# Kernel tuning notes

Hardware: AMD Instinct MI355X
Metric: run time of the kernel (lower is better)

Reference implementation:

```python
import jax, jax.numpy as jnp
import numpy as np

B, S, F, P, D, H, L, FF, R = 64, 4096, 8, 16, 512, 8, 6, 2048, 8
NP = (S - P) // P + 1  # 256 patches (stride == patch_length)
DK = D // H
LORA_SCALING = 16.0 / 8.0  # lora_alpha / lora_rank


def setup_inputs() -> dict:
    key = jax.random.key(0)
    ks = iter(jax.random.split(key, 40))
    def nrm(shape, s=0.02):
        return jax.random.normal(next(ks), shape, jnp.float32) * s
    inp = {
        "x": jax.random.normal(next(ks), (B, S, F), jnp.float32),
        "patch_w": nrm((P * F, D)), "patch_b": jnp.zeros((D,), jnp.float32),
        "patch_ln_w": jnp.ones((D,), jnp.float32), "patch_ln_b": jnp.zeros((D,), jnp.float32),
        "pos_enc": nrm((1, NP, D)),
        "ln1_w": jnp.ones((L, D), jnp.float32), "ln1_b": jnp.zeros((L, D), jnp.float32),
        "q_w": nrm((L, D, D)), "q_b": jnp.zeros((L, D), jnp.float32),
        "k_w": nrm((L, D, D)), "k_b": jnp.zeros((L, D), jnp.float32),
        "v_w": nrm((L, D, D)), "v_b": jnp.zeros((L, D), jnp.float32),
        "lq_down": nrm((L, D, R)), "lq_up": nrm((L, R, D)),
        "lk_down": nrm((L, D, R)), "lk_up": nrm((L, R, D)),
        "lv_down": nrm((L, D, R)), "lv_up": nrm((L, R, D)),
        "o_w": nrm((L, D, D)), "o_b": jnp.zeros((L, D), jnp.float32),
        "ln2_w": jnp.ones((L, D), jnp.float32), "ln2_b": jnp.zeros((L, D), jnp.float32),
        "ff1_w": nrm((L, D, FF)), "ff1_b": jnp.zeros((L, FF), jnp.float32),
        "ff2_w": nrm((L, FF, D)), "ff2_b": jnp.zeros((L, D), jnp.float32),
        "norm_w": jnp.ones((D,), jnp.float32), "norm_b": jnp.zeros((D,), jnp.float32),
    }
    return inp


def _layer_norm(x, w, b):
    m = jnp.mean(x, -1, keepdims=True)
    v = jnp.mean(jnp.square(x - m), -1, keepdims=True)
    return (x - m) * jax.lax.rsqrt(v + 1e-5) * w + b


def _forward(x, patch_w, patch_b, patch_ln_w, patch_ln_b, pos_enc,
             ln1_w, ln1_b, q_w, q_b, k_w, k_b, v_w, v_b,
             lq_down, lq_up, lk_down, lk_up, lv_down, lv_up,
             o_w, o_b, ln2_w, ln2_b, ff1_w, ff1_b, ff2_w, ff2_b,
             norm_w, norm_b):
    # Patch embedding: [B,S,F] -> [B,F,S] -> unfold(stride==patch) -> [B,NP,F*P]
    patches = x.transpose(0, 2, 1).reshape(B, F, NP, P).transpose(0, 2, 1, 3).reshape(B, NP, F * P)
    h = _layer_norm(patches @ patch_w + patch_b, patch_ln_w, patch_ln_b) + pos_enc
    inv_scale = 1.0 / np.sqrt(DK).astype(np.float32)
    for i in range(L):
        y = _layer_norm(h, ln1_w[i], ln1_b[i])
        q = y @ q_w[i] + q_b[i] + (y @ lq_down[i]) @ lq_up[i] * LORA_SCALING
        k = y @ k_w[i] + k_b[i] + (y @ lk_down[i]) @ lk_up[i] * LORA_SCALING
        v = y @ v_w[i] + v_b[i] + (y @ lv_down[i]) @ lv_up[i] * LORA_SCALING
        q = q.reshape(B, NP, H, DK)
        k = k.reshape(B, NP, H, DK)
        v = v.reshape(B, NP, H, DK)
        scores = jnp.einsum('bqhd,bkhd->bhqk', q, k) * inv_scale
        probs = jax.nn.softmax(scores, axis=-1)
        attn = jnp.einsum('bhqk,bkhd->bqhd', probs, v).reshape(B, NP, D)
        h = h + attn @ o_w[i] + o_b[i]
        y = _layer_norm(h, ln2_w[i], ln2_b[i])
        ff = jax.nn.gelu(y @ ff1_w[i] + ff1_b[i], approximate=False) @ ff2_w[i] + ff2_b[i]
        h = h + ff
    h = _layer_norm(h, norm_w, norm_b)
    return h.mean(axis=1)  # [B, D]


def reference(x, patch_w, patch_b, patch_ln_w, patch_ln_b, pos_enc,
              ln1_w, ln1_b, q_w, q_b, k_w, k_b, v_w, v_b,
              lq_down, lq_up, lk_down, lk_up, lv_down, lv_up,
              o_w, o_b, ln2_w, ln2_b, ff1_w, ff1_b, ff2_w, ff2_b,
              norm_w, norm_b):
    return _forward(x, patch_w, patch_b, patch_ln_w, patch_ln_b, pos_enc,
                    ln1_w, ln1_b, q_w, q_b, k_w, k_b, v_w, v_b,
                    lq_down, lq_up, lk_down, lk_up, lv_down, lv_up,
                    o_w, o_b, ln2_w, ln2_b, ff1_w, ff1_b, ff2_w, ff2_b,
                    norm_w, norm_b)
```

## Files before the change

### kernel.cpp

```cpp
#include <hip/hip_runtime.h>
#include <cstdint>
#include <cstddef>

constexpr int BATCH = 64, SEQ = 4096, FEAT = 8, PLEN = 16;
constexpr int DMODEL = 512, NHEAD = 8, NLAYER = 6, DFF = 2048;
constexpr int NPATCH = 256, MROWS = BATCH * NPATCH;
constexpr int DK = 64;
constexpr int LDSP = 72;

typedef unsigned short u16t;
typedef __bf16 bf16t;
typedef bf16t bf16x8 __attribute__((ext_vector_type(8)));
typedef short s16x4 __attribute__((ext_vector_type(4)));
typedef float f32x4 __attribute__((ext_vector_type(4)));

__device__ __forceinline__ float b2f(u16t u) {
  union { unsigned int ui; float f; } v; v.ui = ((unsigned int)u) << 16; return v.f;
}
__device__ __forceinline__ u16t f2b(float f) {
  union { float f; unsigned int ui; } v; v.f = f;
  return (u16t)((v.ui + 0x7fffu + ((v.ui >> 16) & 1u)) >> 16);
}
__device__ __forceinline__ void g2l16(void* lds, const void* g) {
  __builtin_amdgcn_global_load_lds(
      (__attribute__((address_space(1))) void*)g,
      (__attribute__((address_space(3))) void*)lds, 16, 0, 0);
}

__device__ __forceinline__ float gelu_erf(float x) {
  const float z = fabsf(x) * 0.70710678118654752f;
  const float t = __builtin_amdgcn_rcpf(__builtin_fmaf(0.3275911f, z, 1.0f));
  float p = __builtin_fmaf(1.061405429f, t, -1.453152027f);
  p = __builtin_fmaf(p, t, 1.421413741f);
  p = __builtin_fmaf(p, t, -0.284496736f);
  p = __builtin_fmaf(p, t, 0.254829592f);
  const float e = __expf(-z * z);
  const float er = __builtin_fmaf(-p * t, e, 1.0f);
  const float s = copysignf(er, x);
  return 0.5f * x * (1.0f + s);
}

__global__ __launch_bounds__(256, 3) void k_gemm(
    const u16t* __restrict__ A, const u16t* __restrict__ Bt,
    const float* __restrict__ bias, const float* __restrict__ b2,
    const float* __restrict__ b3, float* __restrict__ Cf,
    u16t* __restrict__ Cb, int M, int N, int K, int mode)
{
  __shared__ __align__(16) u16t SH[3 * 8192];

  const int nbn = N >> 7;
  const int cpx = gridDim.x >> 3;
  const int wgid = (blockIdx.x & 7) * cpx + (blockIdx.x >> 3);
  const int bm = (wgid / nbn) << 7;
  const int bn = (wgid % nbn) << 7;

  const int tid = threadIdx.x, wave = tid >> 6, lane = tid & 63;
  const int lr = lane & 15, quad = lane >> 4;
  const int wm = (wave >> 1) << 6;
  const int wn = (wave & 1) << 6;

  const int sseg = (lane & 3) ^ ((lane >> 3) & 3);
  const u16t* gA = A + (size_t)(bm + (lane >> 2)) * K + sseg * 8;
  const u16t* gB = Bt + (size_t)(bn + (lane >> 2)) * K + sseg * 8;

  const int sw8 = (quad ^ ((lr >> 1) & 3)) << 3;
  const int aoff = (wm + lr) * 32 + sw8;
  const int boff = 4096 + (wn + lr) * 32 + sw8;

  f32x4 acc[4][4] = {};

  u16t* buf0 = SH;
  u16t* buf1 = SH + 8192;
  u16t* buf2 = SH + 16384;

#define STAGE(BUF_, S_) do {                                                   \
    g2l16((BUF_) + wave * 512,        gA + (size_t)(wave * 16) * K + (S_) * 32);   \
    g2l16((BUF_) + (wave + 4) * 512,  gA + (size_t)((wave + 4) * 16) * K + (S_) * 32); \
    g2l16((BUF_) + 4096 + wave * 512, gB + (size_t)(wave * 16) * K + (S_) * 32);   \
    g2l16((BUF_) + 4096 + (wave + 4) * 512, gB + (size_t)((wave + 4) * 16) * K + (S_) * 32); \
  } while (0)

  const int nt = K >> 5;
  STAGE(buf0, 0);
  STAGE(buf1, 1);

  for (int t = 0; t < nt - 1; ++t) {
    asm volatile("s_waitcnt vmcnt(4)" ::: "memory");
    __builtin_amdgcn_s_barrier();
    asm volatile("" ::: "memory");
    if (t + 2 < nt) STAGE(buf2, t + 2);
    bf16x8 af[4], bfr[4];
    #pragma unroll
    for (int i = 0; i < 4; ++i) af[i] = *(const bf16x8*)&buf0[aoff + i * 512];
    #pragma unroll
    for (int j = 0; j < 4; ++j) bfr[j] = *(const bf16x8*)&buf0[boff + j * 512];
    __builtin_amdgcn_s_setprio(1);
    #pragma unroll
    for (int j = 0; j < 4; ++j)
      #pragma unroll
      for (int i = 0; i < 4; ++i)
        acc[j][i] = __builtin_amdgcn_mfma_f32_16x16x32_bf16(bfr[j], af[i], acc[j][i], 0, 0, 0);
    __builtin_amdgcn_s_setprio(0);
    u16t* tmp = buf0; buf0 = buf1; buf1 = buf2; buf2 = tmp;
  }
  {
    asm volatile("s_waitcnt vmcnt(0)" ::: "memory");
    __builtin_amdgcn_s_barrier();
    asm volatile("" ::: "memory");
    bf16x8 af[4], bfr[4];
    #pragma unroll
    for (int i = 0; i < 4; ++i) af[i] = *(const bf16x8*)&buf0[aoff + i * 512];
    #pragma unroll
    for (int j = 0; j < 4; ++j) bfr[j] = *(const bf16x8*)&buf0[boff + j * 512];
    __builtin_amdgcn_s_setprio(1);
    #pragma unroll
    for (int j = 0; j < 4; ++j)
      #pragma unroll
      for (int i = 0; i < 4; ++i)
        acc[j][i] = __builtin_amdgcn_mfma_f32_16x16x32_bf16(bfr[j], af[i], acc[j][i], 0, 0, 0);
    __builtin_amdgcn_s_setprio(0);
  }
#undef STAGE

  const float* bp = bias;
  int reg0 = 0;
  if (bias && b2) { reg0 = (bn >> 9) << 9; bp = reg0 == 0 ? bias : (reg0 == 512 ? b2 : b3); }
  float4 bv[4];
  #pragma unroll
  for (int jN = 0; jN < 4; ++jN) {
    const int gn0 = bn + wn + jN * 16 + quad * 4;
    bv[jN] = bias ? *(const float4*)&bp[gn0 - reg0] : make_float4(0.f, 0.f, 0.f, 0.f);
  }

  if (mode <= 1) {
    __syncthreads();
    u16t* E = SH;
    #pragma unroll
    for (int jN = 0; jN < 4; ++jN) {
      const int cl = wn + jN * 16 + quad * 4;
      const int seg = cl >> 3, intra = cl & 7;
      #pragma unroll
      for (int iM = 0; iM < 4; ++iM) {
        const int r = wm + iM * 16 + lr;
        float v0 = acc[jN][iM][0] + bv[jN].x, v1 = acc[jN][iM][1] + bv[jN].y;
        float v2 = acc[jN][iM][2] + bv[jN].z, v3 = acc[jN][iM][3] + bv[jN].w;
        union { u16t h[4]; uint2 u; } pk;
        if (mode == 1) {
          pk.h[0] = f2b(gelu_erf(v0)); pk.h[1] = f2b(gelu_erf(v1));
          pk.h[2] = f2b(gelu_erf(v2)); pk.h[3] = f2b(gelu_erf(v3));
        } else {
          pk.h[0] = f2b(v0); pk.h[1] = f2b(v1); pk.h[2] = f2b(v2); pk.h[3] = f2b(v3);
        }
        *(uint2*)&E[r * 128 + ((seg ^ (r & 7)) << 3) + intra] = pk.u;
      }
    }
    __syncthreads();
    const int rr = tid >> 2, s0 = tid & 3;
    #pragma unroll
    for (int pass = 0; pass < 2; ++pass) {
      const int r = pass * 64 + rr;
      u16t* gout = Cb + (size_t)(bm + r) * N + bn;
      #pragma unroll
      for (int it = 0; it < 4; ++it) {
        const int s = s0 + it * 4;
        uint4 u = *(const uint4*)&E[r * 128 + ((s ^ (r & 7)) << 3)];
        *(uint4*)(gout + s * 8) = u;
      }
    }
  } else {
    #pragma unroll
    for (int jN = 0; jN < 4; ++jN) {
      const int gn0 = bn + wn + jN * 16 + quad * 4;
      #pragma unroll
      for (int iM = 0; iM < 4; ++iM) {
        const int gm = bm + wm + iM * 16 + lr;
        const size_t off = (size_t)gm * N + gn0;
        float v0 = acc[jN][iM][0] + bv[jN].x, v1 = acc[jN][iM][1] + bv[jN].y;
        float v2 = acc[jN][iM][2] + bv[jN].z, v3 = acc[jN][iM][3] + bv[jN].w;
        if (mode == 2) {
          float4 c = *(float4*)(Cf + off);
          c.x += v0; c.y += v1; c.z += v2; c.w += v3;
          *(float4*)(Cf + off) = c;
        } else {
          *(float4*)(Cf + off) = make_float4(v0, v1, v2, v3);
        }
      }
    }
  }
}

__global__ __launch_bounds__(256) void k_prep_w(
    const float* __restrict__ W, const float* __restrict__ down,
    const float* __restrict__ up, u16t* __restrict__ Wt, int K, int N,
    size_t ostride, int orow0)
{
  __shared__ float t[32][33];
  const int z = blockIdx.z;
  const float* Wz = W + (size_t)z * K * N;
  u16t* Wtz = Wt + (size_t)z * ostride + (size_t)orow0 * K;
  const int k0 = blockIdx.x * 32, n0 = blockIdx.y * 32;
  const int tx = threadIdx.x & 31, ty = threadIdx.x >> 5;
  for (int i = ty; i < 32; i += 8) {
    const int kk = k0 + i, nn = n0 + tx;
    float v = Wz[(size_t)kk * N + nn];
    if (down) {
      const float* dz = down + (size_t)z * K * 8 + (size_t)kk * 8;
      const float* uz = up + (size_t)z * 8 * N + nn;
      float lv = 0.f;
      #pragma unroll
      for (int r = 0; r < 8; ++r) lv += dz[r] * uz[(size_t)r * N];
      v += 2.0f * lv;
    }
    t[i][tx] = v;
  }
  __syncthreads();
  for (int i = ty; i < 32; i += 8)
    Wtz[(size_t)(n0 + i) * K + k0 + tx] = f2b(t[tx][i]);
}

__global__ void k_patch(const float* __restrict__ x, u16t* __restrict__ pt) {
  const int idx = blockIdx.x * 256 + threadIdx.x;
  const int col = idx & 127, row = idx >> 7;
  const int f = col >> 4, pp = col & 15;
  const int b = row >> 8, np = row & 255;
  pt[idx] = f2b(x[(((size_t)b << 12) + np * 16 + pp) * 8 + f]);
}

__global__ __launch_bounds__(256) void k_ln(
    const float* __restrict__ xin, const float* __restrict__ w,
    const float* __restrict__ bb, u16t* __restrict__ y)
{
  const int row = blockIdx.x * 4 + (threadIdx.x >> 6);
  const int lane = threadIdx.x & 63;
  const float4* xr = (const float4*)(xin + (size_t)row * 512);
  float4 a = xr[lane * 2], c = xr[lane * 2 + 1];
  float s = a.x + a.y + a.z + a.w + c.x + c.y + c.z + c.w;
  float qq = a.x * a.x + a.y * a.y + a.z * a.z + a.w * a.w +
             c.x * c.x + c.y * c.y + c.z * c.z + c.w * c.w;
  #pragma unroll
  for (int o = 32; o > 0; o >>= 1) { s += __shfl_xor(s, o); qq += __shfl_xor(qq, o); }
  const float mean = s * (1.f / 512.f);
  const float rs = rsqrtf(qq * (1.f / 512.f) - mean * mean + 1e-5f);
  const float4* wr = (const float4*)w; const float4* br = (const float4*)bb;
  float4 w0 = wr[lane * 2], w1 = wr[lane * 2 + 1];
  float4 b0 = br[lane * 2], b1 = br[lane * 2 + 1];
  union { u16t h[8]; uint4 v; } pk;
  pk.h[0] = f2b((a.x - mean) * rs * w0.x + b0.x);
  pk.h[1] = f2b((a.y - mean) * rs * w0.y + b0.y);
  pk.h[2] = f2b((a.z - mean) * rs * w0.z + b0.z);
  pk.h[3] = f2b((a.w - mean) * rs * w0.w + b0.w);
  pk.h[4] = f2b((c.x - mean) * rs * w1.x + b1.x);
  pk.h[5] = f2b((c.y - mean) * rs * w1.y + b1.y);
  pk.h[6] = f2b((c.z - mean) * rs * w1.z + b1.z);
  pk.h[7] = f2b((c.w - mean) * rs * w1.w + b1.w);
  *(uint4*)(y + (size_t)row * 512 + lane * 8) = pk.v;
}

__global__ __launch_bounds__(256) void k_ln_pos(
    const float* __restrict__ xin, const float* __restrict__ w,
    const float* __restrict__ bb, const float* __restrict__ pos,
    float* __restrict__ h)
{
  const int row = blockIdx.x * 4 + (threadIdx.x >> 6);
  const int lane = threadIdx.x & 63;
  const float4* xr = (const float4*)(xin + (size_t)row * 512);
  float4 a = xr[lane * 2], c = xr[lane * 2 + 1];
  float s = a.x + a.y + a.z + a.w + c.x + c.y + c.z + c.w;
  float qq = a.x * a.x + a.y * a.y + a.z * a.z + a.w * a.w +
             c.x * c.x + c.y * c.y + c.z * c.z + c.w * c.w;
  #pragma unroll
  for (int o = 32; o > 0; o >>= 1) { s += __shfl_xor(s, o); qq += __shfl_xor(qq, o); }
  const float mean = s * (1.f / 512.f);
  const float rs = rsqrtf(qq * (1.f / 512.f) - mean * mean + 1e-5f);
  const float4* wr = (const float4*)w; const float4* br = (const float4*)bb;
  float4 w0 = wr[lane * 2], w1 = wr[lane * 2 + 1];
  float4 b0 = br[lane * 2], b1 = br[lane * 2 + 1];
  const int np = row & 255;
  const float4* pr = (const float4*)(pos + (size_t)np * 512);
  float4 p0 = pr[lane * 2], p1 = pr[lane * 2 + 1];
  float4 o0, o1;
  o0.x = (a.x - mean) * rs * w0.x + b0.x + p0.x;
  o0.y = (a.y - mean) * rs * w0.y + b0.y + p0.y;
  o0.z = (a.z - mean) * rs * w0.z + b0.z + p0.z;
  o0.w = (a.w - mean) * rs * w0.w + b0.w + p0.w;
  o1.x = (c.x - mean) * rs * w1.x + b1.x + p1.x;
  o1.y = (c.y - mean) * rs * w1.y + b1.y + p1.y;
  o1.z = (c.z - mean) * rs * w1.z + b1.z + p1.z;
  o1.w = (c.w - mean) * rs * w1.w + b1.w + p1.w;
  float4* hr = (float4*)(h + (size_t)row * 512);
  hr[lane * 2] = o0; hr[lane * 2 + 1] = o1;
}

__global__ __launch_bounds__(256) void k_attn(
    const u16t* __restrict__ qkv, u16t* __restrict__ out)
{
  __shared__ __align__(16) u16t Qs[128 * LDSP];
  __shared__ __align__(16) u16t Ks[64 * LDSP];
  __shared__ __align__(16) u16t Vts[64 * LDSP];

  const int bh = blockIdx.x >> 1, half = blockIdx.x & 1;
  const int b = bh >> 3, hd = bh & 7;
  const int tid = threadIdx.x, wave = tid >> 6, lane = tid & 63;
  const int lr = lane & 15, quad = lane >> 4;

  const size_t rowbase = (size_t)b * 256;
  const u16t* qg = qkv + (rowbase + half * 128) * 1536 + hd * 64;
  const u16t* kg = qkv + rowbase * 1536 + 512 + hd * 64;
  const u16t* vg = qkv + rowbase * 1536 + 1024 + hd * 64;

  #pragma unroll
  for (int i = 0; i < 4; ++i) {
    const int idx = tid + i * 256, row = idx >> 3, seg = idx & 7;
    uint4 u = *(const uint4*)(qg + (size_t)row * 1536 + seg * 8);
    *(uint4*)&Qs[row * LDSP + seg * 8] = u;
  }
  __syncthreads();

  bf16x8 qf[2][2];
  #pragma unroll
  for (int qi = 0; qi < 2; ++qi)
    #pragma unroll
    for (int dh = 0; dh < 2; ++dh)
      qf[qi][dh] = *(const bf16x8*)&Qs[(wave * 32 + qi * 16 + lr) * LDSP + dh * 32 + quad * 8];

  f32x4 O[2][4] = {};
  float mrun[2] = {-1e30f, -1e30f}, lrun[2] = {0.f, 0.f};

  for (int c = 0; c < 4; ++c) {
    __syncthreads();
    #pragma unroll
    for (int i = 0; i < 2; ++i) {
      const int idx = tid + i * 256, row = idx >> 3, seg = idx & 7;
      uint4 u = *(const uint4*)(kg + (size_t)(c * 64 + row) * 1536 + seg * 8);
      *(uint4*)&Ks[row * LDSP + seg * 8] = u;
    }
    {
      const int key = tid & 63, dg = (tid >> 6) * 16;
      const u16t* vrow = vg + (size_t)(c * 64 + key) * 1536 + dg;
      union { u16t h[16]; uint4 v[2]; } tmp;
      tmp.v[0] = *(const uint4*)(vrow);
      tmp.v[1] = *(const uint4*)(vrow + 8);
      #pragma unroll
      for (int i = 0; i < 16; ++i)
        Vts[(dg + i) * LDSP + key] = tmp.h[i];
    }
    __syncthreads();

    #pragma unroll
    for (int qi = 0; qi < 2; ++qi) {
      f32x4 s[4];
      #pragma unroll
      for (int kt = 0; kt < 4; ++kt) {
        f32x4 a = {};
        #pragma unroll
        for (int dh = 0; dh < 2; ++dh) {
          bf16x8 kf = *(const bf16x8*)&Ks[(kt * 16 + lr) * LDSP + dh * 32 + quad * 8];
          a = __builtin_amdgcn_mfma_f32_16x16x32_bf16(kf, qf[qi][dh], a, 0, 0, 0);
        }
        s[kt] = a;
      }
      constexpr float SC = 0.125f * 1.44269504088896f;
      float cmax = -1e30f;
      #pragma unroll
      for (int kt = 0; kt < 4; ++kt)
        #pragma unroll
        for (int r = 0; r < 4; ++r) { s[kt][r] *= SC; cmax = fmaxf(cmax, s[kt][r]); }
      cmax = fmaxf(cmax, __shfl_xor(cmax, 16));
      cmax = fmaxf(cmax, __shfl_xor(cmax, 32));
      const float mn = fmaxf(mrun[qi], cmax);
      const float alpha = exp2f(mrun[qi] - mn);
      mrun[qi] = mn;
      float lsum = 0.f;
      s16x4 pf[4];
      #pragma unroll
      for (int kt = 0; kt < 4; ++kt) {
        #pragma unroll
        for (int r = 0; r < 4; ++r) {
          const u16t eb = f2b(exp2f(s[kt][r] - mn));
          pf[kt][r] = (short)eb;
          lsum += b2f(eb);
        }
      }
      lsum += __shfl_xor(lsum, 16);
      lsum += __shfl_xor(lsum, 32);
      lrun[qi] = lrun[qi] * alpha + lsum;
      #pragma unroll
      for (int dt = 0; dt < 4; ++dt) {
        f32x4 o = O[qi][dt];
        o[0] *= alpha; o[1] *= alpha; o[2] *= alpha; o[3] *= alpha;
        #pragma unroll
        for (int kt = 0; kt < 4; ++kt) {
          s16x4 vf = *(const s16x4*)&Vts[(dt * 16 + lr) * LDSP + kt * 16 + quad * 4];
          o = __builtin_amdgcn_mfma_f32_16x16x16bf16_1k(vf, pf[kt], o, 0, 0, 0);
        }
        O[qi][dt] = o;
      }
    }
  }
  #pragma unroll
  for (int qi = 0; qi < 2; ++qi) {
    const float rl = 1.f / lrun[qi];
    u16t* orow = out + (rowbase + half * 128 + wave * 32 + qi * 16 + lr) * 512 + hd * 64 + quad * 4;
    #pragma unroll
    for (int dt = 0; dt < 4; ++dt) {
      union { u16t h[4]; uint2 v; } pk;
      #pragma unroll
      for (int r = 0; r < 4; ++r) pk.h[r] = f2b(O[qi][dt][r] * rl);
      *(uint2*)(orow + dt * 16) = pk.v;
    }
  }
}

__global__ void k_mean(const u16t* __restrict__ y, float* __restrict__ out) {
  const int b = blockIdx.x, d = threadIdx.x;
  float s = 0.f;
  #pragma unroll 8
  for (int np = 0; np < 256; ++np) s += b2f(y[((size_t)b * 256 + np) * 512 + d]);
  out[(size_t)b * 512 + d] = s * (1.f / 256.f);
}

extern "C" void kernel_launch(void* const* d_in, const int* in_sizes, int n_in,
                              void* d_out, int out_size, void* d_ws, size_t ws_size,
                              hipStream_t stream)
{
  (void)in_sizes; (void)n_in; (void)out_size;
  const float* x        = (const float*)d_in[0];
  const float* patch_w  = (const float*)d_in[1];
  const float* patch_b  = (const float*)d_in[2];
  const float* patch_ln_w = (const float*)d_in[3];
  const float* patch_ln_b = (const float*)d_in[4];
  const float* pos_enc  = (const float*)d_in[5];
  const float* ln1_w    = (const float*)d_in[6];
  const float* ln1_b    = (const float*)d_in[7];
  const float* q_w      = (const float*)d_in[8];
  const float* q_b      = (const float*)d_in[9];
  const float* k_w      = (const float*)d_in[10];
  const float* k_b      = (const float*)d_in[11];
  const float* v_w      = (const float*)d_in[12];
  const float* v_b      = (const float*)d_in[13];
  const float* lq_down  = (const float*)d_in[14];
  const float* lq_up    = (const float*)d_in[15];
  const float* lk_down  = (const float*)d_in[16];
  const float* lk_up    = (const float*)d_in[17];
  const float* lv_down  = (const float*)d_in[18];
  const float* lv_up    = (const float*)d_in[19];
  const float* o_w      = (const float*)d_in[20];
  const float* o_b      = (const float*)d_in[21];
  const float* ln2_w    = (const float*)d_in[22];
  const float* ln2_b    = (const float*)d_in[23];
  const float* ff1_w    = (const float*)d_in[24];
  const float* ff1_b    = (const float*)d_in[25];
  const float* ff2_w    = (const float*)d_in[26];
  const float* ff2_b    = (const float*)d_in[27];
  const float* norm_w   = (const float*)d_in[28];
  const float* norm_b   = (const float*)d_in[29];
  float* out = (float*)d_out;

  char* p = (char*)d_ws;
  float* h  = (float*)p;  p += (size_t)MROWS * 512 * 4;
  u16t*  y  = (u16t*)p;   p += (size_t)MROWS * 512 * 2;
  char* uni = p;          p += (size_t)4 * MROWS * 512 * 2;
  u16t* qkvb = (u16t*)uni;
  u16t* ab = (u16t*)(uni + (size_t)MROWS * 1536 * 2);
  u16t* g  = (u16t*)uni;
  float* pe = (float*)uni;
  u16t* pt = (u16t*)(uni + (size_t)MROWS * 512 * 4);
  u16t* wqkv = (u16t*)p; p += (size_t)NLAYER * 1536 * 512 * 2;
  u16t* wo = (u16t*)p; p += (size_t)NLAYER * 512 * 512 * 2;
  u16t* w1 = (u16t*)p; p += (size_t)NLAYER * 512 * 2048 * 2;
  u16t* w2 = (u16t*)p; p += (size_t)NLAYER * 2048 * 512 * 2;
  u16t* wp = (u16t*)p; p += (size_t)512 * 128 * 2;
  if ((size_t)(p - (char*)d_ws) > ws_size) return;

  const dim3 blk(256);
  const size_t QKVS = (size_t)1536 * 512;
  k_prep_w<<<dim3(16, 16, NLAYER), blk, 0, stream>>>(q_w, lq_down, lq_up, wqkv, 512, 512, QKVS, 0);
  k_prep_w<<<dim3(16, 16, NLAYER), blk, 0, stream>>>(k_w, lk_down, lk_up, wqkv, 512, 512, QKVS, 512);
  k_prep_w<<<dim3(16, 16, NLAYER), blk, 0, stream>>>(v_w, lv_down, lv_up, wqkv, 512, 512, QKVS, 1024);
  k_prep_w<<<dim3(16, 16, NLAYER), blk, 0, stream>>>(o_w, nullptr, nullptr, wo, 512, 512, (size_t)512 * 512, 0);
  k_prep_w<<<dim3(16, 64, NLAYER), blk, 0, stream>>>(ff1_w, nullptr, nullptr, w1, 512, 2048, (size_t)512 * 2048, 0);
  k_prep_w<<<dim3(64, 16, NLAYER), blk, 0, stream>>>(ff2_w, nullptr, nullptr, w2, 2048, 512, (size_t)2048 * 512, 0);
  k_prep_w<<<dim3(4, 16, 1),       blk, 0, stream>>>(patch_w, nullptr, nullptr, wp, 128, 512, 0, 0);

  k_patch<<<dim3(MROWS * 128 / 256), blk, 0, stream>>>(x, pt);
  k_gemm<<<dim3(128 * 4), blk, 0, stream>>>(pt, wp, patch_b, nullptr, nullptr, pe, nullptr, MROWS, 512, 128, 3);
  k_ln_pos<<<dim3(MROWS / 4), blk, 0, stream>>>(pe, patch_ln_w, patch_ln_b, pos_enc, h);

  for (int i = 0; i < NLAYER; ++i) {
    const size_t ws512 = (size_t)i * 512 * 512, wsff = (size_t)i * 512 * 2048;
    k_ln<<<dim3(MROWS / 4), blk, 0, stream>>>(h, ln1_w + i * 512, ln1_b + i * 512, y);
    k_gemm<<<dim3(128 * 12), blk, 0, stream>>>(y, wqkv + i * QKVS, q_b + i * 512, k_b + i * 512,
                                               v_b + i * 512, nullptr, qkvb, MROWS, 1536, 512, 0);
    k_attn<<<dim3(1024), blk, 0, stream>>>(qkvb, ab);
    k_gemm<<<dim3(128 * 4), blk, 0, stream>>>(ab, wo + ws512, o_b + i * 512, nullptr, nullptr, h, nullptr, MROWS, 512, 512, 2);
    k_ln<<<dim3(MROWS / 4), blk, 0, stream>>>(h, ln2_w + i * 512, ln2_b + i * 512, y);
    k_gemm<<<dim3(128 * 16), blk, 0, stream>>>(y, w1 + wsff, ff1_b + i * 2048, nullptr, nullptr, nullptr, g, MROWS, 2048, 512, 1);
    k_gemm<<<dim3(128 * 4), blk, 0, stream>>>(g, w2 + wsff, ff2_b + i * 512, nullptr, nullptr, h, nullptr, MROWS, 512, 2048, 2);
  }
  k_ln<<<dim3(MROWS / 4), blk, 0, stream>>>(h, norm_w, norm_b, y);
  k_mean<<<dim3(BATCH), dim3(512), 0, stream>>>(y, out);
}
```

Before: 1.482 ms.

## Add 256x128-tile GEMM with triple-buffered LDS for FF1 projection

Adds a new GEMM kernel that uses 256x128 output tiles, with each wave computing 128x64 through an 8x4 MFMA accumulator array. It stages A and B through a three-deep LDS ring using direct global-to-LDS loads, and raises instruction priority around the MFMA block. The FF1 GEMM (N=2048, with a GELU epilogue) now uses this kernel, which halves the block count and raises operand reuse per loaded tile. The cost is much higher register and LDS pressure: 128 accumulator floats per thread and 72KB of LDS per block, which may cap occupancy at two blocks per CU.

Result: no change. 1.469 ms (-0.9%).

```diff
diff --git a/kernel.cpp b/kernel.cpp
--- a/kernel.cpp
+++ b/kernel.cpp
@@ -173,6 +173,157 @@
       const int gn0 = bn + wn + jN * 16 + quad * 4;
       #pragma unroll
       for (int iM = 0; iM < 4; ++iM) {
+        const int gm = bm + wm + iM * 16 + lr;
+        const size_t off = (size_t)gm * N + gn0;
+        float v0 = acc[jN][iM][0] + bv[jN].x, v1 = acc[jN][iM][1] + bv[jN].y;
+        float v2 = acc[jN][iM][2] + bv[jN].z, v3 = acc[jN][iM][3] + bv[jN].w;
+        if (mode == 2) {
+          float4 c = *(float4*)(Cf + off);
+          c.x += v0; c.y += v1; c.z += v2; c.w += v3;
+          *(float4*)(Cf + off) = c;
+        } else {
+          *(float4*)(Cf + off) = make_float4(v0, v1, v2, v3);
+        }
+      }
+    }
+  }
+}
+
+__global__ __launch_bounds__(256, 2) void k_gemmw(
+    const u16t* __restrict__ A, const u16t* __restrict__ Bt,
+    const float* __restrict__ bias, const float* __restrict__ b2,
+    const float* __restrict__ b3, float* __restrict__ Cf,
+    u16t* __restrict__ Cb, int M, int N, int K, int mode)
+{
+  __shared__ __align__(16) u16t SH[3 * 12288];
+
+  const int nbn = N >> 7;
+  const int cpx = gridDim.x >> 3;
+  const int wgid = (blockIdx.x & 7) * cpx + (blockIdx.x >> 3);
+  const int bm = (wgid / nbn) << 8;
+  const int bn = (wgid % nbn) << 7;
+
+  const int tid = threadIdx.x, wave = tid >> 6, lane = tid & 63;
+  const int lr = lane & 15, quad = lane >> 4;
+  const int wm = (wave >> 1) << 7;
+  const int wn = (wave & 1) << 6;
+
+  const int sseg = (lane & 3) ^ ((lane >> 3) & 3);
+  const u16t* gA = A + (size_t)(bm + (lane >> 2)) * K + sseg * 8;
+  const u16t* gB = Bt + (size_t)(bn + (lane >> 2)) * K + sseg * 8;
+
+  const int sw8 = (quad ^ ((lr >> 1) & 3)) << 3;
+  const int aoff = (wm + lr) * 32 + sw8;
+  const int boff = 8192 + (wn + lr) * 32 + sw8;
+
+  f32x4 acc[4][8] = {};
+
+  u16t* buf0 = SH;
+  u16t* buf1 = SH + 12288;
+  u16t* buf2 = SH + 24576;
+
+#define STAGE_W(BUF_, S_) do {                                                 \
+    g2l16((BUF_) + wave * 512,        gA + (size_t)(wave * 16) * K + (S_) * 32);   \
+    g2l16((BUF_) + (wave + 4) * 512,  gA + (size_t)((wave + 4) * 16) * K + (S_) * 32); \
+    g2l16((BUF_) + (wave + 8) * 512,  gA + (size_t)((wave + 8) * 16) * K + (S_) * 32); \
+    g2l16((BUF_) + (wave + 12) * 512, gA + (size_t)((wave + 12) * 16) * K + (S_) * 32); \
+    g2l16((BUF_) + 8192 + wave * 512, gB + (size_t)(wave * 16) * K + (S_) * 32);   \
+    g2l16((BUF_) + 8192 + (wave + 4) * 512, gB + (size_t)((wave + 4) * 16) * K + (S_) * 32); \
+  } while (0)
+
+  const int nt = K >> 5;
+  STAGE_W(buf0, 0);
+  STAGE_W(buf1, 1);
+
+  for (int t = 0; t < nt - 1; ++t) {
+    asm volatile("s_waitcnt vmcnt(6)" ::: "memory");
+    __builtin_amdgcn_s_barrier();
+    asm volatile("" ::: "memory");
+    if (t + 2 < nt) STAGE_W(buf2, t + 2);
+    bf16x8 af[8], bfr[4];
+    #pragma unroll
+    for (int i = 0; i < 8; ++i) af[i] = *(const bf16x8*)&buf0[aoff + i * 512];
+    #pragma unroll
+    for (int j = 0; j < 4; ++j) bfr[j] = *(const bf16x8*)&buf0[boff + j * 512];
+    __builtin_amdgcn_s_setprio(1);
+    #pragma unroll
+    for (int j = 0; j < 4; ++j)
+      #pragma unroll
+      for (int i = 0; i < 8; ++i)
+        acc[j][i] = __builtin_amdgcn_mfma_f32_16x16x32_bf16(bfr[j], af[i], acc[j][i], 0, 0, 0);
+    __builtin_amdgcn_s_setprio(0);
+    u16t* tmp = buf0; buf0 = buf1; buf1 = buf2; buf2 = tmp;
+  }
+  {
+    asm volatile("s_waitcnt vmcnt(0)" ::: "memory");
+    __builtin_amdgcn_s_barrier();
+    asm volatile("" ::: "memory");
+    bf16x8 af[8], bfr[4];
+    #pragma unroll
+    for (int i = 0; i < 8; ++i) af[i] = *(const bf16x8*)&buf0[aoff + i * 512];
+    #pragma unroll
+    for (int j = 0; j < 4; ++j) bfr[j] = *(const bf16x8*)&buf0[boff + j * 512];
+    __builtin_amdgcn_s_setprio(1);
+    #pragma unroll
+    for (int j = 0; j < 4; ++j)
+      #pragma unroll
+      for (int i = 0; i < 8; ++i)
+        acc[j][i] = __builtin_amdgcn_mfma_f32_16x16x32_bf16(bfr[j], af[i], acc[j][i], 0, 0, 0);
+    __builtin_amdgcn_s_setprio(0);
+  }
+#undef STAGE_W
+
+  const float* bp = bias;
+  int reg0 = 0;
+  if (bias && b2) { reg0 = (bn >> 9) << 9; bp = reg0 == 0 ? bias : (reg0 == 512 ? b2 : b3); }
+  float4 bv[4];
+  #pragma unroll
+  for (int jN = 0; jN < 4; ++jN) {
+    const int gn0 = bn + wn + jN * 16 + quad * 4;
+    bv[jN] = bias ? *(const float4*)&bp[gn0 - reg0] : make_float4(0.f, 0.f, 0.f, 0.f);
+  }
+
+  if (mode <= 1) {
+    __syncthreads();
+    u16t* E = SH;
+    #pragma unroll
+    for (int jN = 0; jN < 4; ++jN) {
+      const int cl = wn + jN * 16 + quad * 4;
+      const int seg = cl >> 3, intra = cl & 7;
+      #pragma unroll
+      for (int iM = 0; iM < 8; ++iM) {
+        const int r = wm + iM * 16 + lr;
+        float v0 = acc[jN][iM][0] + bv[jN].x, v1 = acc[jN][iM][1] + bv[jN].y;
+        float v2 = acc[jN][iM][2] + bv[jN].z, v3 = acc[jN][iM][3] + bv[jN].w;
+        union { u16t h[4]; uint2 u; } pk;
+        if (mode == 1) {
+          pk.h[0] = f2b(gelu_erf(v0)); pk.h[1] = f2b(gelu_erf(v1));
+          pk.h[2] = f2b(gelu_erf(v2)); pk.h[3] = f2b(gelu_erf(v3));
+        } else {
+          pk.h[0] = f2b(v0); pk.h[1] = f2b(v1); pk.h[2] = f2b(v2); pk.h[3] = f2b(v3);
+        }
+        *(uint2*)&E[r * 128 + ((seg ^ (r & 7)) << 3) + intra] = pk.u;
+      }
+    }
+    __syncthreads();
+    const int rr = tid >> 2, s0 = tid & 3;
+    #pragma unroll
+    for (int pass = 0; pass < 4; ++pass) {
+      const int r = pass * 64 + rr;
+      u16t* gout = Cb + (size_t)(bm + r) * N + bn;
+      #pragma unroll
+      for (int it = 0; it < 4; ++it) {
+        const int s = s0 + it * 4;
+        uint4 u = *(const uint4*)&E[r * 128 + ((s ^ (r & 7)) << 3)];
+        *(uint4*)(gout + s * 8) = u;
+      }
+    }
+  } else {
+    #pragma unroll
+    for (int jN = 0; jN < 4; ++jN) {
+      const int gn0 = bn + wn + jN * 16 + quad * 4;
+      #pragma unroll
+      for (int iM = 0; iM < 8; ++iM) {
         const int gm = bm + wm + iM * 16 + lr;
         const size_t off = (size_t)gm * N + gn0;
         float v0 = acc[jN][iM][0] + bv[jN].x, v1 = acc[jN][iM][1] + bv[jN].y;
@@ -494,7 +645,7 @@
     k_attn<<<dim3(1024), blk, 0, stream>>>(qkvb, ab);
     k_gemm<<<dim3(128 * 4), blk, 0, stream>>>(ab, wo + ws512, o_b + i * 512, nullptr, nullptr, h, nullptr, MROWS, 512, 512, 2);
     k_ln<<<dim3(MROWS / 4), blk, 0, stream>>>(h, ln2_w + i * 512, ln2_b + i * 512, y);
-    k_gemm<<<dim3(128 * 16), blk, 0, stream>>>(y, w1 + wsff, ff1_b + i * 2048, nullptr, nullptr, nullptr, g, MROWS, 2048, 512, 1);
+    k_gemmw<<<dim3(64 * 16), blk, 0, stream>>>(y, w1 + wsff, ff1_b + i * 2048, nullptr, nullptr, nullptr, g, MROWS, 2048, 512, 1);
     k_gemm<<<dim3(128 * 4), blk, 0, stream>>>(g, w2 + wsff, ff2_b + i * 512, nullptr, nullptr, h, nullptr, MROWS, 512, 2048, 2);
   }
   k_ln<<<dim3(MROWS / 4), blk, 0, stream>>>(h, norm_w, norm_b, y);
```
